# Kernel tuning notes

Hardware: AMD Instinct MI355X
Metric: run time of the kernel (lower is better)

Reference implementation:

```python
import jax, jax.numpy as jnp
from jax import lax
import numpy as np

B, S, G = 64, 200, 8
CHAR_V, GAZ_V = 8000, 100000
D_CHAR, D_GAZ, H = 128, 128, 512
N_LABEL = 20
N_TAG = N_LABEL + 2  # CRF adds START (N_TAG-2) and STOP (N_TAG-1)


def setup_inputs() -> dict:
    key = jax.random.key(0)
    ks = jax.random.split(key, 16)
    lengths = jax.random.randint(ks[0], (B,), S // 2, S + 1)
    pos = jnp.arange(S)[None, :]
    mask = pos < lengths[:, None]
    char_inputs = jax.random.randint(ks[1], (B, S), 0, CHAR_V)
    gaz_ids = jax.random.randint(ks[2], (B, S, G), 0, GAZ_V)
    cnt = jax.random.randint(ks[3], (B, S), 1, G + 1)
    gaz_mask = (jnp.arange(G)[None, None, :] < cnt[..., None]).astype(jnp.int32)
    rev_gaz_ids = jax.random.randint(ks[4], (B, S, G), 0, GAZ_V)
    rcnt = jax.random.randint(ks[5], (B, S), 1, G + 1)
    rev_gaz_mask = (jnp.arange(G)[None, None, :] < rcnt[..., None]).astype(jnp.int32)
    sc = 0.1
    D_in = D_CHAR + D_GAZ
    return dict(
        char_inputs=char_inputs, lengths=lengths, mask=mask,
        gaz_ids=gaz_ids, gaz_mask=gaz_mask,
        rev_gaz_ids=rev_gaz_ids, rev_gaz_mask=rev_gaz_mask,
        char_table=jax.random.normal(ks[6], (CHAR_V, D_CHAR)) * sc,
        gaz_table=jax.random.normal(ks[7], (GAZ_V, D_GAZ)) * sc,
        w_ih_f=jax.random.normal(ks[8], (4 * H, D_in)) * sc,
        w_hh_f=jax.random.normal(ks[9], (4 * H, H)) * sc,
        b_f=jnp.zeros((4 * H,), jnp.float32),
        w_ih_b=jax.random.normal(ks[10], (4 * H, D_in)) * sc,
        w_hh_b=jax.random.normal(ks[11], (4 * H, H)) * sc,
        b_b=jnp.zeros((4 * H,), jnp.float32),
        W_out=jax.random.normal(ks[12], (2 * H, N_TAG)) * sc,
        b_out=jnp.zeros((N_TAG,), jnp.float32),
        transitions=jax.random.normal(ks[13], (N_TAG, N_TAG)) * sc,
    )


def rev_pad(x, lengths):
    # reverse each sequence within its valid length (reverse_padded_sequence)
    b, s = x.shape[0], x.shape[1]
    pos = jnp.arange(s)[None, :]
    idx = jnp.where(pos < lengths[:, None], lengths[:, None] - 1 - pos, pos)
    idx = idx.reshape((b, s) + (1,) * (x.ndim - 2))
    return jnp.take_along_axis(x, jnp.broadcast_to(idx, x.shape), axis=1)


def gaz_embed(table, ids, m):
    # masked mean over the G candidate gaz words per char (Gaz_Embed, type=1)
    e = table[ids]                                   # [B,S,G,D]
    mf = m.astype(e.dtype)[..., None]
    return (e * mf).sum(2) / jnp.maximum(mf.sum(2), 1.0)


def lstm(x, w_ih, w_hh, b):
    # x: [B,S,D]; torch gate order i,f,g,o
    h0 = jnp.zeros((x.shape[0], H), x.dtype)

    def step(carry, xt):
        h, c = carry
        g = xt @ w_ih.T + h @ w_hh.T + b
        i, f, gg, o = jnp.split(g, 4, axis=-1)
        c = jax.nn.sigmoid(f) * c + jax.nn.sigmoid(i) * jnp.tanh(gg)
        h = jax.nn.sigmoid(o) * jnp.tanh(c)
        return (h, c), h

    _, hs = lax.scan(step, (h0, h0), x.transpose(1, 0, 2))
    return hs.transpose(1, 0, 2)                     # [B,S,H]


def emissions_fn(char_inputs, lengths, gaz_ids, gaz_mask, rev_gaz_ids, rev_gaz_mask,
                 char_table, gaz_table, w_ih_f, w_hh_f, b_f, w_ih_b, w_hh_b, b_b,
                 W_out, b_out):
    char_embs = char_table[char_inputs]              # [B,S,Dc]
    rev_char_embs = rev_pad(char_embs, lengths)
    g_f = gaz_embed(gaz_table, gaz_ids, gaz_mask)
    g_b = gaz_embed(gaz_table, rev_pad(rev_gaz_ids, lengths), rev_pad(rev_gaz_mask, lengths))
    fwd_in = jnp.concatenate([char_embs, g_f], axis=-1)
    bwd_in = jnp.concatenate([rev_char_embs, g_b], axis=-1)
    h_f = lstm(fwd_in, w_ih_f, w_hh_f, b_f)
    h_b = rev_pad(lstm(bwd_in, w_ih_b, w_hh_b, b_b), lengths)
    lstm_outs = jnp.concatenate([h_f, h_b], axis=-1)  # [B,S,2H]
    return lstm_outs @ W_out + b_out                  # [B,S,N_TAG]


def viterbi(emissions, mask, transitions):
    # transitions[prev, next]; START=N_TAG-2, STOP=N_TAG-1
    n = emissions.shape[-1]
    start, stop = n - 2, n - 1
    init = emissions[:, 0] + transitions[start][None, :]     # [B,n]
    ident = jnp.arange(n, dtype=jnp.int32)[None, :]

    def vstep(part, inp):
        emit_t, m_t = inp                                    # [B,n], [B]
        cand = part[:, :, None] + transitions[None] + emit_t[:, None, :]
        new = cand.max(axis=1)
        bp = cand.argmax(axis=1).astype(jnp.int32)
        part = jnp.where(m_t[:, None], new, part)
        bp = jnp.where(m_t[:, None], bp, ident)              # identity bp on pad
        return part, bp

    part, bps = lax.scan(vstep, init,
                         (emissions[:, 1:].transpose(1, 0, 2), mask[:, 1:].T))
    last_tag = (part + transitions[:, stop][None, :]).argmax(-1).astype(jnp.int32)

    def btstep(tag, bp):
        prev = jnp.take_along_axis(bp, tag[:, None], axis=1)[:, 0]
        return prev, prev

    _, prev_tags = lax.scan(btstep, last_tag, bps, reverse=True)  # [S-1,B]
    tags = jnp.concatenate([prev_tags.T, last_tag[:, None]], axis=1)
    return tags * mask.astype(tags.dtype)


def reference(char_inputs, lengths, mask, gaz_ids, gaz_mask, rev_gaz_ids, rev_gaz_mask,
              char_table, gaz_table, w_ih_f, w_hh_f, b_f, w_ih_b, w_hh_b, b_b,
              W_out, b_out, transitions):
    emissions = emissions_fn(char_inputs, lengths, gaz_ids, gaz_mask,
                             rev_gaz_ids, rev_gaz_mask, char_table, gaz_table,
                             w_ih_f, w_hh_f, b_f, w_ih_b, w_hh_b, b_b, W_out, b_out)
    return viterbi(emissions, mask, transitions)
```

## Files before the change

kernel.cpp:

```cpp
#include <hip/hip_runtime.h>
#include <math.h>

#define S_LEN 200
#define BATCH 64
#define HID   512
#define NTAG  22
#define TCH   25
#define MC    (TCH*BATCH)

typedef unsigned short u16;
typedef unsigned int   u32;

__device__ __forceinline__ float bf2f(u16 u){
  union { u32 ui; float f; } v; v.ui = ((u32)u) << 16; return v.f;
}

__global__ void k_detect(const u32* __restrict__ w, int* __restrict__ flag){
  __shared__ int cnt;
  if (threadIdx.x == 0) cnt = 0;
  __syncthreads();
  int hits = 0;
  for (int i = threadIdx.x; i < 16384; i += 256){
    u32 e = (w[i] & 0x7F80u);
    if (e >= 0x3800u && e <= 0x4080u) hits++;
  }
  atomicAdd(&cnt, hits);
  __syncthreads();
  if (threadIdx.x == 0) *flag = (cnt > 8192) ? 1 : 0;
}

__global__ void k_cvt_f(const void* __restrict__ src, float* __restrict__ dst,
                        int n, const int* __restrict__ flag){
  int i = blockIdx.x*blockDim.x + threadIdx.x;
  if (i >= n) return;
  if (*flag) dst[i] = bf2f(((const u16*)src)[i]);
  else       dst[i] = ((const float*)src)[i];
}

__global__ void k_cvt_wt(const void* __restrict__ src, float* __restrict__ dst,
                         const int* __restrict__ flag){
  int i = blockIdx.x*blockDim.x + threadIdx.x;
  if (i >= 1024*24) return;
  int k = i / 24, tag = i % 24;
  float v = 0.f;
  if (tag < NTAG){
    v = (*flag) ? bf2f(((const u16*)src)[k*NTAG + tag])
                : ((const float*)src)[k*NTAG + tag];
  }
  int half = k >> 9, kk = k & 511;
  dst[((size_t)half*512 + kk)*24 + tag] = v;
}

__global__ void k_zero(float* __restrict__ p, int n){
  int i = blockIdx.x*blockDim.x + threadIdx.x;
  if (i < n) p[i] = 0.f;
}

__global__ __launch_bounds__(128)
void k_build(const int* __restrict__ ci, const int* __restrict__ lengths,
             const int* __restrict__ gid, const int* __restrict__ gm,
             const int* __restrict__ rgid, const int* __restrict__ rgm,
             const void* __restrict__ ctab, const void* __restrict__ gtab,
             const int* __restrict__ flag,
             float* __restrict__ fin, float* __restrict__ bin)
{
  int bs = blockIdx.x;
  int b = bs / S_LEN, s = bs % S_LEN;
  int d = threadIdx.x;
  int isbf = *flag;
  int len = lengths[b];
  int sb = (s < len) ? (len - 1 - s) : s;
  size_t orow = ((size_t)s*BATCH + b)*256;

  {
    int cid = ci[bs];
    float cv = isbf ? bf2f(((const u16*)ctab)[(size_t)cid*128 + d])
                    : ((const float*)ctab)[(size_t)cid*128 + d];
    fin[orow + d] = cv;
    const int* gg = gid + (size_t)bs*8;
    const int* mm = gm  + (size_t)bs*8;
    float sum = 0.f, cntf = 0.f;
    for (int g = 0; g < 8; ++g){
      float m = (float)mm[g];
      int gw = gg[g];
      float gv = isbf ? bf2f(((const u16*)gtab)[(size_t)gw*128 + d])
                      : ((const float*)gtab)[(size_t)gw*128 + d];
      sum += m * gv; cntf += m;
    }
    fin[orow + 128 + d] = sum / fmaxf(cntf, 1.f);
  }
  {
    int bsr = b*S_LEN + sb;
    int cid = ci[bsr];
    float cv = isbf ? bf2f(((const u16*)ctab)[(size_t)cid*128 + d])
                    : ((const float*)ctab)[(size_t)cid*128 + d];
    bin[orow + d] = cv;
    const int* gg = rgid + (size_t)bsr*8;
    const int* mm = rgm  + (size_t)bsr*8;
    float sum = 0.f, cntf = 0.f;
    for (int g = 0; g < 8; ++g){
      float m = (float)mm[g];
      int gw = gg[g];
      float gv = isbf ? bf2f(((const u16*)gtab)[(size_t)gw*128 + d])
                      : ((const float*)gtab)[(size_t)gw*128 + d];
      sum += m * gv; cntf += m;
    }
    bin[orow + 128 + d] = sum / fmaxf(cntf, 1.f);
  }
}

__global__ __launch_bounds__(256)
void k_gemm_ih(const float* __restrict__ Af, const float* __restrict__ Ab,
               const float* __restrict__ wih,
               const float* __restrict__ bias,
               float* __restrict__ gxc,
               int t0)
{
  const int dir = blockIdx.z;
  const float* A = (dir ? Ab : Af) + (size_t)t0*BATCH*256;
  const float* W = wih + (size_t)dir*2048*256;
  const float* bi = bias + (size_t)dir*2048;
  float* C = gxc + (size_t)dir*2048*MC;
  const int m0 = blockIdx.y * 64;
  const int n0 = blockIdx.x * 64;
  const int tid = threadIdx.x;
  __shared__ float As[32][64];
  __shared__ float Ws[32][64];
  const int lr = tid >> 2;
  const int kq = (tid & 3) * 8;
  const int tx = tid & 15;
  const int ty = tid >> 4;
  float acc[4][4] = {};

  for (int k0 = 0; k0 < 256; k0 += 32){
    float4 a0 = *(const float4*)(A + (size_t)(m0+lr)*256 + k0 + kq);
    float4 a1 = *(const float4*)(A + (size_t)(m0+lr)*256 + k0 + kq + 4);
    float4 w0 = *(const float4*)(W + (size_t)(n0+lr)*256 + k0 + kq);
    float4 w1 = *(const float4*)(W + (size_t)(n0+lr)*256 + k0 + kq + 4);
    As[kq+0][lr]=a0.x; As[kq+1][lr]=a0.y; As[kq+2][lr]=a0.z; As[kq+3][lr]=a0.w;
    As[kq+4][lr]=a1.x; As[kq+5][lr]=a1.y; As[kq+6][lr]=a1.z; As[kq+7][lr]=a1.w;
    Ws[kq+0][lr]=w0.x; Ws[kq+1][lr]=w0.y; Ws[kq+2][lr]=w0.z; Ws[kq+3][lr]=w0.w;
    Ws[kq+4][lr]=w1.x; Ws[kq+5][lr]=w1.y; Ws[kq+6][lr]=w1.z; Ws[kq+7][lr]=w1.w;
    __syncthreads();
    #pragma unroll 8
    for (int kk = 0; kk < 32; ++kk){
      float4 av = *(const float4*)(&As[kk][ty*4]);
      float4 wv = *(const float4*)(&Ws[kk][tx*4]);
      acc[0][0]+=av.x*wv.x; acc[0][1]+=av.x*wv.y; acc[0][2]+=av.x*wv.z; acc[0][3]+=av.x*wv.w;
      acc[1][0]+=av.y*wv.x; acc[1][1]+=av.y*wv.y; acc[1][2]+=av.y*wv.z; acc[1][3]+=av.y*wv.w;
      acc[2][0]+=av.z*wv.x; acc[2][1]+=av.z*wv.y; acc[2][2]+=av.z*wv.z; acc[2][3]+=av.z*wv.w;
      acc[3][0]+=av.w*wv.x; acc[3][1]+=av.w*wv.y; acc[3][2]+=av.w*wv.z; acc[3][3]+=av.w*wv.w;
    }
    __syncthreads();
  }

  #pragma unroll
  for (int j = 0; j < 4; ++j){
    float bj = bi[n0 + tx*4 + j];
    float4 o = make_float4(acc[0][j]+bj, acc[1][j]+bj, acc[2][j]+bj, acc[3][j]+bj);
    *(float4*)(C + (size_t)(n0 + tx*4 + j)*MC + m0 + ty*4) = o;
  }
}

__global__ __launch_bounds__(512)
void k_step(const float* __restrict__ whh,
            const float* __restrict__ gxc,
            float* __restrict__ hbuf,
            float* __restrict__ cbuf,
            float* __restrict__ hseq,
            int t, int tc)
{
  const int dir = blockIdx.y;
  const int hrow_base = blockIdx.x * 4;
  const int tid = threadIdx.x;
  const int b = tid & 63;
  const int uw = __builtin_amdgcn_readfirstlane(tid >> 6);
  const int uk0 = uw * 64;

  __shared__ float part[8*16*64];

  const float* hprev = hbuf + (size_t)(dir*2 + (t&1))*HID*BATCH;
  float* hnext       = hbuf + (size_t)(dir*2 + ((t+1)&1))*HID*BATCH;
  const float* whhd  = whh + (size_t)dir*2048*512;

  float hv[64];
  #pragma unroll
  for (int j = 0; j < 64; ++j)
    hv[j] = hprev[(size_t)(uk0 + j)*BATCH + b];

  float acc[16];
  #pragma unroll
  for (int r = 0; r < 16; ++r) acc[r] = 0.f;

  #pragma unroll
  for (int r = 0; r < 16; ++r){
    const int row_glob = (r >> 2)*512 + hrow_base + (r & 3);
    const float* wr = whhd + (size_t)row_glob*512 + uk0;
    #pragma unroll
    for (int j = 0; j < 64; ++j)
      acc[r] += wr[j] * hv[j];
  }

  #pragma unroll
  for (int r = 0; r < 16; ++r)
    part[(uw*16 + r)*64 + b] = acc[r];
  __syncthreads();

  if (tid < 256){
    const int hr = tid >> 6;
    const int bb = tid & 63;
    const int hrow = hrow_base + hr;
    float g4[4];
    #pragma unroll
    for (int g = 0; g < 4; ++g){
      const int r = g*4 + hr;
      float s = 0.f;
      #pragma unroll
      for (int ww = 0; ww < 8; ++ww)
        s += part[(ww*16 + r)*64 + bb];
      g4[g] = s;
    }
    const float* gxb = gxc + (size_t)dir*2048*MC + (size_t)tc*BATCH + bb;
    float gi = g4[0] + gxb[(size_t)(   0 + hrow)*MC];
    float gf = g4[1] + gxb[(size_t)( 512 + hrow)*MC];
    float gg = g4[2] + gxb[(size_t)(1024 + hrow)*MC];
    float go = g4[3] + gxb[(size_t)(1536 + hrow)*MC];
    float si = 1.f/(1.f+expf(-gi));
    float sf = 1.f/(1.f+expf(-gf));
    float so = 1.f/(1.f+expf(-go));
    size_t ci_ = ((size_t)dir*HID + hrow)*BATCH + bb;
    float c = cbuf[ci_];
    c = sf*c + si*tanhf(gg);
    float h = so*tanhf(c);
    cbuf[ci_] = c;
    hnext[(size_t)hrow*BATCH + bb] = h;
    hseq[(((size_t)dir*S_LEN + t)*HID + hrow)*BATCH + bb] = h;
  }
}

__global__ __launch_bounds__(256)
void k_emis(const float* __restrict__ hseq, const int* __restrict__ lengths,
            const float* __restrict__ wpad,
            const float* __restrict__ bout,
            float* __restrict__ emisF, float* __restrict__ emisB)
{
  const int t = blockIdx.x;
  const int dir = blockIdx.y;
  const int tid = threadIdx.x;
  const int b = tid & 63;
  const int utg = __builtin_amdgcn_readfirstlane(tid >> 6);

  __shared__ float hl[64*64];

  const float* hsrc = hseq + ((size_t)(dir*S_LEN + t)*HID)*BATCH;
  const float* wbase = wpad + (size_t)dir*512*24 + utg*6;

  float acc[6] = {0.f,0.f,0.f,0.f,0.f,0.f};

  for (int c = 0; c < 8; ++c){
    const float4* s4 = (const float4*)(hsrc + (size_t)c*64*64);
    float4* d4 = (float4*)hl;
    #pragma unroll
    for (int q = 0; q < 4; ++q) d4[q*256 + tid] = s4[q*256 + tid];
    __syncthreads();
    const float* wrow = wbase + (size_t)c*64*24;
    #pragma unroll 4
    for (int k = 0; k < 64; ++k){
      float hval = hl[k*64 + b];
      #pragma unroll
      for (int i = 0; i < 6; ++i) acc[i] += hval * wrow[k*24 + i];
    }
    __syncthreads();
  }

  const int len = lengths[b];
  const int pos = dir ? ((t < len) ? (len - 1 - t) : t) : t;
  float* dst = (dir ? emisB : emisF) + ((size_t)b*S_LEN + pos)*NTAG;
  #pragma unroll
  for (int i = 0; i < 6; ++i){
    int tag = utg*6 + i;
    if (tag < NTAG) dst[tag] = acc[i] + (dir ? 0.f : bout[tag]);
  }
}

__global__ __launch_bounds__(64)
void k_viterbi(const float* __restrict__ emisF, const float* __restrict__ emisB,
               const int* __restrict__ lengths,
               const float* __restrict__ trans, int* __restrict__ out)
{
  int b = blockIdx.x;
  int j = threadIdx.x;
  __shared__ float tr[NTAG*NTAG];
  __shared__ float part[NTAG];
  __shared__ unsigned char bp[(S_LEN-1)*NTAG];
  for (int i = j; i < NTAG*NTAG; i += 64) tr[i] = trans[i];
  int len = lengths[b];
  const float* ef = emisF + (size_t)b*S_LEN*NTAG;
  const float* eb = emisB + (size_t)b*S_LEN*NTAG;
  __syncthreads();
  if (j < NTAG) part[j] = ef[j] + eb[j] + tr[(NTAG-2)*NTAG + j];
  __syncthreads();
  for (int t = 1; t < S_LEN; ++t){
    float best = -3.4e38f; int bi = 0;
    if (j < NTAG){
      float e = ef[t*NTAG + j] + eb[t*NTAG + j];
      for (int i = 0; i < NTAG; ++i){
        float v = part[i] + tr[i*NTAG + j] + e;
        if (v > best){ best = v; bi = i; }
      }
    }
    __syncthreads();
    if (j < NTAG){
      if (t < len){ part[j] = best; bp[(t-1)*NTAG + j] = (unsigned char)bi; }
      else        { bp[(t-1)*NTAG + j] = (unsigned char)j; }
    }
    __syncthreads();
  }
  if (j == 0){
    float best = -3.4e38f; int tag = 0;
    for (int i = 0; i < NTAG; ++i){
      float v = part[i] + tr[i*NTAG + (NTAG-1)];
      if (v > best){ best = v; tag = i; }
    }
    out[b*S_LEN + S_LEN-1] = (S_LEN-1 < len) ? tag : 0;
    for (int t = S_LEN-2; t >= 0; --t){
      tag = bp[t*NTAG + tag];
      out[b*S_LEN + t] = (t < len) ? tag : 0;
    }
  }
}

extern "C" void kernel_launch(void* const* d_in, const int* in_sizes, int n_in,
                              void* d_out, int out_size, void* d_ws, size_t ws_size,
                              hipStream_t stream)
{
  (void)in_sizes; (void)n_in; (void)out_size; (void)ws_size;
  const int* char_inputs  = (const int*)d_in[0];
  const int* lengths      = (const int*)d_in[1];
  const int* gaz_ids      = (const int*)d_in[3];
  const int* gaz_mask     = (const int*)d_in[4];
  const int* rev_gaz_ids  = (const int*)d_in[5];
  const int* rev_gaz_mask = (const int*)d_in[6];
  const void* char_table  = d_in[7];
  const void* gaz_table   = d_in[8];
  const void* w_ih_f = d_in[9];
  const void* w_hh_f = d_in[10];
  const void* b_f    = d_in[11];
  const void* w_ih_b = d_in[12];
  const void* w_hh_b = d_in[13];
  const void* b_b    = d_in[14];
  const void* W_out  = d_in[15];
  const void* b_out  = d_in[16];
  const void* trans  = d_in[17];

  char* ws = (char*)d_ws;
  size_t off = 0;
  auto alloc = [&](size_t bytes)->char*{
    char* p = ws + off; off = (off + bytes + 255) & ~(size_t)255; return p;
  };
  int*   flag   = (int*)  alloc(256);
  float* whh32  = (float*)alloc(2ull*2048*512*4);
  float* wih32  = (float*)alloc(2ull*2048*256*4);
  float* bias32 = (float*)alloc(2ull*2048*4);
  float* wpad   = (float*)alloc(2ull*512*24*4);
  float* bout32 = (float*)alloc(22ull*4);
  float* trans32= (float*)alloc(484ull*4);
  float* fwd_in = (float*)alloc(12800ull*256*4);
  float* bwd_in = (float*)alloc(12800ull*256*4);
  float* gxc    = (float*)alloc(2ull*2048*MC*4);
  float* hbuf   = (float*)alloc(2ull*2*512*64*4);
  float* cbuf   = (float*)alloc(2ull*512*64*4);
  float* hseq   = (float*)alloc(2ull*200*512*64*4);
  float* emisF  = (float*)alloc(12800ull*22*4);
  float* emisB  = (float*)alloc(12800ull*22*4);

  k_detect<<<1,256,0,stream>>>((const u32*)char_table, flag);
  k_cvt_f<<<4096,256,0,stream>>>(w_hh_f, whh32,           1048576, flag);
  k_cvt_f<<<4096,256,0,stream>>>(w_hh_b, whh32 + 1048576, 1048576, flag);
  k_cvt_f<<<2048,256,0,stream>>>(w_ih_f, wih32,            524288, flag);
  k_cvt_f<<<2048,256,0,stream>>>(w_ih_b, wih32 + 524288,   524288, flag);
  k_cvt_f<<<8,256,0,stream>>>(b_f, bias32,        2048, flag);
  k_cvt_f<<<8,256,0,stream>>>(b_b, bias32 + 2048, 2048, flag);
  k_cvt_wt<<<96,256,0,stream>>>(W_out, wpad, flag);
  k_cvt_f<<<1,256,0,stream>>>(b_out, bout32, 22, flag);
  k_cvt_f<<<2,256,0,stream>>>(trans, trans32, 484, flag);

  k_build<<<12800,128,0,stream>>>(char_inputs, lengths, gaz_ids, gaz_mask,
                                  rev_gaz_ids, rev_gaz_mask, char_table, gaz_table,
                                  flag, fwd_in, bwd_in);

  k_zero<<<768,256,0,stream>>>(hbuf, 2*2*512*64 + 2*512*64);

  for (int t0 = 0; t0 < S_LEN; t0 += TCH){
    k_gemm_ih<<<dim3(32,TCH,2),256,0,stream>>>(fwd_in, bwd_in, wih32, bias32,
                                               gxc, t0);
    for (int tc = 0; tc < TCH; ++tc)
      k_step<<<dim3(128,2),512,0,stream>>>(whh32, gxc, hbuf, cbuf, hseq, t0+tc, tc);
  }

  k_emis<<<dim3(S_LEN,2),256,0,stream>>>(hseq, lengths, wpad, bout32, emisF, emisB);
  k_viterbi<<<64,64,0,stream>>>(emisF, emisB, lengths, trans32, (int*)d_out);
}
```

Measured before the change: 2.822 ms.

## Enlarge input-projection GEMM tiles, chunk more timesteps, and restructure Viterbi recursion

The input-to-hidden GEMM moves from 64x64 tiles with 4x4 per-thread outputs to 128x128 tiles with 8x8 per-thread outputs and padded shared memory, which raises arithmetic intensity and cuts bank conflicts. The time chunk grows from 25 to 40 steps, so fewer GEMM launches are needed, at the cost of a larger gate buffer. The Viterbi kernel keeps each tag's transition column in registers, double-buffers the partial scores to drop one barrier per step, and uses a tree argmax. The 8x8 accumulators raise register pressure and the larger tiles give fewer blocks, while the sequential per-step kernel launches, which likely dominate, are unchanged.

```diff
diff --git a/kernel.cpp b/kernel.cpp
--- a/kernel.cpp
+++ b/kernel.cpp
@@ -5,7 +5,7 @@
 #define BATCH 64
 #define HID   512
 #define NTAG  22
-#define TCH   25
+#define TCH   40
 #define MC    (TCH*BATCH)
 
 typedef unsigned short u16;
@@ -121,44 +121,58 @@
   const float* W = wih + (size_t)dir*2048*256;
   const float* bi = bias + (size_t)dir*2048;
   float* C = gxc + (size_t)dir*2048*MC;
-  const int m0 = blockIdx.y * 64;
-  const int n0 = blockIdx.x * 64;
+  const int m0 = blockIdx.y * 128;
+  const int n0 = blockIdx.x * 128;
   const int tid = threadIdx.x;
-  __shared__ float As[32][64];
-  __shared__ float Ws[32][64];
-  const int lr = tid >> 2;
-  const int kq = (tid & 3) * 8;
+
+  __shared__ float As[32][132];
+  __shared__ float Ws[32][132];
+
+  const int lrow = tid >> 3;
+  const int lk   = (tid & 7) * 4;
+
   const int tx = tid & 15;
   const int ty = tid >> 4;
-  float acc[4][4] = {};
+
+  float acc[8][8] = {};
 
   for (int k0 = 0; k0 < 256; k0 += 32){
-    float4 a0 = *(const float4*)(A + (size_t)(m0+lr)*256 + k0 + kq);
-    float4 a1 = *(const float4*)(A + (size_t)(m0+lr)*256 + k0 + kq + 4);
-    float4 w0 = *(const float4*)(W + (size_t)(n0+lr)*256 + k0 + kq);
-    float4 w1 = *(const float4*)(W + (size_t)(n0+lr)*256 + k0 + kq + 4);
-    As[kq+0][lr]=a0.x; As[kq+1][lr]=a0.y; As[kq+2][lr]=a0.z; As[kq+3][lr]=a0.w;
-    As[kq+4][lr]=a1.x; As[kq+5][lr]=a1.y; As[kq+6][lr]=a1.z; As[kq+7][lr]=a1.w;
-    Ws[kq+0][lr]=w0.x; Ws[kq+1][lr]=w0.y; Ws[kq+2][lr]=w0.z; Ws[kq+3][lr]=w0.w;
-    Ws[kq+4][lr]=w1.x; Ws[kq+5][lr]=w1.y; Ws[kq+6][lr]=w1.z; Ws[kq+7][lr]=w1.w;
+    #pragma unroll
+    for (int q = 0; q < 4; ++q){
+      const int row = lrow + q*32;
+      float4 a = *(const float4*)(A + (size_t)(m0+row)*256 + k0 + lk);
+      float4 w = *(const float4*)(W + (size_t)(n0+row)*256 + k0 + lk);
+      As[lk+0][row]=a.x; As[lk+1][row]=a.y; As[lk+2][row]=a.z; As[lk+3][row]=a.w;
+      Ws[lk+0][row]=w.x; Ws[lk+1][row]=w.y; Ws[lk+2][row]=w.z; Ws[lk+3][row]=w.w;
+    }
     __syncthreads();
     #pragma unroll 8
     for (int kk = 0; kk < 32; ++kk){
-      float4 av = *(const float4*)(&As[kk][ty*4]);
-      float4 wv = *(const float4*)(&Ws[kk][tx*4]);
-      acc[0][0]+=av.x*wv.x; acc[0][1]+=av.x*wv.y; acc[0][2]+=av.x*wv.z; acc[0][3]+=av.x*wv.w;
-      acc[1][0]+=av.y*wv.x; acc[1][1]+=av.y*wv.y; acc[1][2]+=av.y*wv.z; acc[1][3]+=av.y*wv.w;
-      acc[2][0]+=av.z*wv.x; acc[2][1]+=av.z*wv.y; acc[2][2]+=av.z*wv.z; acc[2][3]+=av.z*wv.w;
-      acc[3][0]+=av.w*wv.x; acc[3][1]+=av.w*wv.y; acc[3][2]+=av.w*wv.z; acc[3][3]+=av.w*wv.w;
+      float4 a0 = *(const float4*)(&As[kk][ty*8]);
+      float4 a1 = *(const float4*)(&As[kk][ty*8+4]);
+      float4 w0 = *(const float4*)(&Ws[kk][tx*8]);
+      float4 w1 = *(const float4*)(&Ws[kk][tx*8+4]);
+      float am[8] = {a0.x,a0.y,a0.z,a0.w,a1.x,a1.y,a1.z,a1.w};
+      float wn[8] = {w0.x,w0.y,w0.z,w0.w,w1.x,w1.y,w1.z,w1.w};
+      #pragma unroll
+      for (int i = 0; i < 8; ++i)
+        #pragma unroll
+        for (int jj = 0; jj < 8; ++jj)
+          acc[i][jj] += am[i]*wn[jj];
     }
     __syncthreads();
   }
 
   #pragma unroll
-  for (int j = 0; j < 4; ++j){
-    float bj = bi[n0 + tx*4 + j];
-    float4 o = make_float4(acc[0][j]+bj, acc[1][j]+bj, acc[2][j]+bj, acc[3][j]+bj);
-    *(float4*)(C + (size_t)(n0 + tx*4 + j)*MC + m0 + ty*4) = o;
+  for (int jj = 0; jj < 8; ++jj){
+    const int n = n0 + tx*8 + jj;
+    const float bj = bi[n];
+    #pragma unroll
+    for (int i = 0; i < 8; i += 4){
+      float4 o = make_float4(acc[i][jj]+bj, acc[i+1][jj]+bj,
+                             acc[i+2][jj]+bj, acc[i+3][jj]+bj);
+      *(float4*)(C + (size_t)n*MC + m0 + ty*8 + i) = o;
+    }
   }
 }
 
@@ -288,39 +302,70 @@
                const int* __restrict__ lengths,
                const float* __restrict__ trans, int* __restrict__ out)
 {
-  int b = blockIdx.x;
-  int j = threadIdx.x;
-  __shared__ float tr[NTAG*NTAG];
-  __shared__ float part[NTAG];
+  const int b = blockIdx.x;
+  const int j = threadIdx.x;
+  __shared__ float part[2][NTAG];
   __shared__ unsigned char bp[(S_LEN-1)*NTAG];
-  for (int i = j; i < NTAG*NTAG; i += 64) tr[i] = trans[i];
-  int len = lengths[b];
+  const int len = lengths[b];
   const float* ef = emisF + (size_t)b*S_LEN*NTAG;
   const float* eb = emisB + (size_t)b*S_LEN*NTAG;
+
+  float trr[NTAG];
+  if (j < NTAG){
+    #pragma unroll
+    for (int i = 0; i < NTAG; ++i) trr[i] = trans[i*NTAG + j];
+    part[0][j] = ef[j] + eb[j] + trans[(NTAG-2)*NTAG + j];
+  }
   __syncthreads();
-  if (j < NTAG) part[j] = ef[j] + eb[j] + tr[(NTAG-2)*NTAG + j];
-  __syncthreads();
+
   for (int t = 1; t < S_LEN; ++t){
-    float best = -3.4e38f; int bi = 0;
+    const int cur = (t-1) & 1, nxt = t & 1;
     if (j < NTAG){
-      float e = ef[t*NTAG + j] + eb[t*NTAG + j];
-      for (int i = 0; i < NTAG; ++i){
-        float v = part[i] + tr[i*NTAG + j] + e;
-        if (v > best){ best = v; bi = i; }
+      float v[NTAG];
+      #pragma unroll
+      for (int i = 0; i < NTAG; ++i) v[i] = part[cur][i] + trr[i];
+      float m1[11]; int x1[11];
+      #pragma unroll
+      for (int i = 0; i < 11; ++i){
+        const bool g = v[2*i+1] > v[2*i];
+        m1[i] = g ? v[2*i+1] : v[2*i];
+        x1[i] = g ? 2*i+1 : 2*i;
       }
+      float m2[6]; int x2[6];
+      #pragma unroll
+      for (int i = 0; i < 5; ++i){
+        const bool g = m1[2*i+1] > m1[2*i];
+        m2[i] = g ? m1[2*i+1] : m1[2*i];
+        x2[i] = g ? x1[2*i+1] : x1[2*i];
+      }
+      m2[5] = m1[10]; x2[5] = x1[10];
+      float m3[3]; int x3[3];
+      #pragma unroll
+      for (int i = 0; i < 3; ++i){
+        const bool g = m2[2*i+1] > m2[2*i];
+        m3[i] = g ? m2[2*i+1] : m2[2*i];
+        x3[i] = g ? x2[2*i+1] : x2[2*i];
+      }
+      const bool g01 = m3[1] > m3[0];
+      float mm = g01 ? m3[1] : m3[0];
+      int   xx = g01 ? x3[1] : x3[0];
+      const bool g2 = m3[2] > mm;
+      mm = g2 ? m3[2] : mm;
+      xx = g2 ? x3[2] : xx;
+
+      const float e = ef[t*NTAG + j] + eb[t*NTAG + j];
+      if (t < len){ part[nxt][j] = mm + e; bp[(t-1)*NTAG + j] = (unsigned char)xx; }
+      else        { part[nxt][j] = part[cur][j]; bp[(t-1)*NTAG + j] = (unsigned char)j; }
     }
     __syncthreads();
-    if (j < NTAG){
-      if (t < len){ part[j] = best; bp[(t-1)*NTAG + j] = (unsigned char)bi; }
-      else        { bp[(t-1)*NTAG + j] = (unsigned char)j; }
-    }
-    __syncthreads();
-  }
+  }
+
   if (j == 0){
+    const int fin = (S_LEN-1) & 1;
     float best = -3.4e38f; int tag = 0;
     for (int i = 0; i < NTAG; ++i){
-      float v = part[i] + tr[i*NTAG + (NTAG-1)];
-      if (v > best){ best = v; tag = i; }
+      float vv = part[fin][i] + trans[i*NTAG + (NTAG-1)];
+      if (vv > best){ best = vv; tag = i; }
     }
     out[b*S_LEN + S_LEN-1] = (S_LEN-1 < len) ? tag : 0;
     for (int t = S_LEN-2; t >= 0; --t){
@@ -392,8 +437,8 @@
   k_zero<<<768,256,0,stream>>>(hbuf, 2*2*512*64 + 2*512*64);
 
   for (int t0 = 0; t0 < S_LEN; t0 += TCH){
-    k_gemm_ih<<<dim3(32,TCH,2),256,0,stream>>>(fwd_in, bwd_in, wih32, bias32,
-                                               gxc, t0);
+    k_gemm_ih<<<dim3(16,MC/128,2),256,0,stream>>>(fwd_in, bwd_in, wih32, bias32,
+                                                  gxc, t0);
     for (int tc = 0; tc < TCH; ++tc)
       k_step<<<dim3(128,2),512,0,stream>>>(whh32, gxc, hbuf, cbuf, hseq, t0+tc, tc);
   }
```

After: 2.805 ms. About the same (-0.6%).
